# Kernel optimization log

Measured on AMD Instinct MI355X. Metric: run time of the kernel, lower is better.

The kernel has to match this reference:

```python
import jax, jax.numpy as jnp
import numpy as np

B, T, IN_DIM, EMBED, OUT_DIM, WS = 32, 512, 2048, 512, 29, 64


def setup_inputs() -> dict:
    key = jax.random.key(0)
    ks = jax.random.split(key, 8)
    x = jax.random.normal(ks[0], (B, T, IN_DIM), dtype=jnp.float32)
    # pack_padded_sequence contract: lengths sorted descending, max length == T
    lens = jnp.sort(jax.random.randint(ks[1], (B,), T // 2, T + 1))[::-1]
    sample_lengths = lens.at[0].set(T).astype(jnp.int64)
    s_in = 1.0 / np.sqrt(IN_DIM)
    s_q = 1.0 / np.sqrt(OUT_DIM)
    s_o = 1.0 / np.sqrt(EMBED)
    return {
        "x": x,
        "sample_lengths": sample_lengths,
        "W_in": jax.random.normal(ks[2], (IN_DIM, EMBED), jnp.float32) * s_in,
        "b_in": jnp.zeros((EMBED,), jnp.float32),
        "W_q": jax.random.normal(ks[3], (OUT_DIM, EMBED), jnp.float32) * s_q,
        "b_q": jnp.zeros((EMBED,), jnp.float32),
        "W_out": jax.random.normal(ks[4], (EMBED, OUT_DIM), jnp.float32) * s_o,
        "b_out": jnp.zeros((OUT_DIM,), jnp.float32),
        "window_size": WS,
    }


def reference(x, sample_lengths, W_in, b_in, W_q, b_q, W_out, b_out, window_size):
    # x: [B, T, input_dim] padded (pad_packed_sequence equivalent)
    Bb, Tt, _ = x.shape
    D = W_in.shape[1]
    h = x @ W_in + b_in                       # input_proj, [B, T, D]
    lens = sample_lengths
    j = jnp.arange(Tt)
    scale = 1.0 / jnp.sqrt(jnp.asarray(D, h.dtype))
    neg = jnp.finfo(h.dtype).min
    # generate_query0 with init_strategy='fix': ones, last channel = 9
    q0 = jnp.ones((Bb, 1, W_q.shape[0]), h.dtype).at[:, :, -1].set(9.0)

    def step(query, t):
        q = query @ W_q + b_q                 # query_proj, [B, 1, D]
        scores = jnp.einsum('bod,btd->bot', q, h) * scale  # [B, 1, T]
        # local window around query index t, clipped to each sequence length
        valid = (j >= t - window_size) & (j <= t + window_size) & (j[None, :] < lens[:, None])
        w = jax.nn.softmax(jnp.where(valid[:, None, :], scores, neg), axis=-1)
        alive = (t < lens).astype(h.dtype)[:, None, None]  # finished seqs -> zeros (blank_out/blank_wgts)
        out = jnp.einsum('bot,btd->bod', w, h) * alive      # [B, 1, D]
        new_query = out @ W_out + b_out        # output_proj, [B, 1, 29]
        return new_query, (new_query[:, 0, :], (w * alive)[:, 0, :])

    _, (outs, wgts) = jax.lax.scan(step, q0, jnp.arange(Tt))
    outputs = jnp.transpose(outs, (1, 0, 2))   # [B, T, 29]
    weights = jnp.transpose(wgts, (1, 0, 2))   # [B, T, T]
    return outputs, weights
```

## Files before the change

### kernel.cpp

```cpp
#include <hip/hip_runtime.h>
#include <math.h>

#define BB 32
#define TT 512
#define IND 2048
#define DD 512
#define OD 29
#define WCOLS 64
#define GC 32
#define PTK 116
#define PTB 18560

typedef float v2f __attribute__((ext_vector_type(2)));

__device__ __forceinline__ v2f pk_fma(v2f a, v2f b, v2f c) {
  v2f d;
  asm("v_pk_fma_f32 %0, %1, %2, %3" : "=v"(d) : "v"(a), "v"(b), "v"(c));
  return d;
}

template<int CTRL, int RM>
__device__ __forceinline__ float updpp(float idv, float x) {
  return __int_as_float(__builtin_amdgcn_update_dpp(
      __float_as_int(idv), __float_as_int(x), CTRL, RM, 0xf, false));
}

__device__ __forceinline__ float red_max64(float x) {
  const float ID = -3.0e38f;
  x = fmaxf(x, updpp<0xB1, 0xf>(ID, x));
  x = fmaxf(x, updpp<0x4E, 0xf>(ID, x));
  x = fmaxf(x, updpp<0x124, 0xf>(ID, x));
  x = fmaxf(x, updpp<0x128, 0xf>(ID, x));
  x = fmaxf(x, updpp<0x142, 0xa>(ID, x));
  x = fmaxf(x, updpp<0x143, 0xc>(ID, x));
  return __int_as_float(__builtin_amdgcn_readlane(__float_as_int(x), 63));
}

__device__ __forceinline__ float red_sum64(float x) {
  x += updpp<0xB1, 0xf>(0.f, x);
  x += updpp<0x4E, 0xf>(0.f, x);
  x += updpp<0x124, 0xf>(0.f, x);
  x += updpp<0x128, 0xf>(0.f, x);
  x += updpp<0x142, 0xa>(0.f, x);
  x += updpp<0x143, 0xc>(0.f, x);
  return __int_as_float(__builtin_amdgcn_readlane(__float_as_int(x), 63));
}

__global__ void k_zero(float* __restrict__ p, int n) {
  int n4 = n >> 2;
  int i = blockIdx.x * blockDim.x + threadIdx.x;
  int stride = gridDim.x * blockDim.x;
  float4 z = make_float4(0.f, 0.f, 0.f, 0.f);
  for (int j = i; j < n4; j += stride) ((float4*)p)[j] = z;
  int base = (n4 << 2) + i;
  if (base < n) p[base] = 0.f;
}

__global__ __launch_bounds__(64) void k_transform(
    const float* __restrict__ W_in, const float* __restrict__ b_in,
    const float* __restrict__ W_q,  const float* __restrict__ b_q,
    const float* __restrict__ W_out, float* __restrict__ Wt) {
  int i = blockIdx.x;
  int c = threadIdx.x;
  const float* row = (i < IND) ? (W_in + (size_t)i * DD) : b_in;
  const float* m;
  int strd;
  bool valid = true, dscale = false;
  if (c < OD)                { m = W_q + (size_t)c * DD; strd = 1; dscale = true; }
  else if (c == OD)          { m = b_q;                  strd = 1; dscale = true; }
  else if (c >= 32 && c < 32 + OD) { m = W_out + (c - 32); strd = OD; }
  else                       { m = b_q; strd = 0; valid = false; }
  float a0 = 0.f, a1 = 0.f, a2 = 0.f, a3 = 0.f;
  for (int d = 0; d < DD; d += 4) {
    a0 += row[d + 0] * m[(size_t)(d + 0) * strd];
    a1 += row[d + 1] * m[(size_t)(d + 1) * strd];
    a2 += row[d + 2] * m[(size_t)(d + 2) * strd];
    a3 += row[d + 3] * m[(size_t)(d + 3) * strd];
  }
  float acc = (a0 + a1) + (a2 + a3);
  if (dscale) acc *= (1.0f / sqrtf((float)DD));
  if (!valid) acc = 0.f;
  Wt[(size_t)i * WCOLS + c] = acc;
}

__global__ __launch_bounds__(256) void k_gemm(
    const float* __restrict__ x, const float* __restrict__ Wt,
    float* __restrict__ GPC, float* __restrict__ Ptg) {
  __shared__ float xt[128][65];
  int tid = threadIdx.x;
  int r = tid & 63;
  int cg16 = __builtin_amdgcn_readfirstlane((tid >> 6) << 4);
  int m0 = blockIdx.x << 6;
  int lr = tid >> 2, lc = tid & 3;
  const float* xl = x + (size_t)(m0 + lr) * IND;
  float4 a0 = make_float4(0,0,0,0), a1 = a0, a2 = a0, a3 = a0;
  for (int kk = 0; kk < IND; kk += 128) {
    __syncthreads();
    #pragma unroll
    for (int j = 0; j < 8; ++j) {
      int k = (lc + 4 * j) << 2;
      float4 v = *(const float4*)(xl + kk + k);
      xt[k + 0][lr] = v.x; xt[k + 1][lr] = v.y;
      xt[k + 2][lr] = v.z; xt[k + 3][lr] = v.w;
    }
    __syncthreads();
    const float* wb = Wt + (size_t)kk * WCOLS + cg16;
    #pragma unroll 4
    for (int k = 0; k < 128; ++k) {
      float xv = xt[k][r];
      const float* wk = wb + (size_t)k * WCOLS;
      float4 w0 = *(const float4*)(wk + 0);
      float4 w1 = *(const float4*)(wk + 4);
      float4 w2 = *(const float4*)(wk + 8);
      float4 w3 = *(const float4*)(wk + 12);
      a0.x += xv * w0.x; a0.y += xv * w0.y; a0.z += xv * w0.z; a0.w += xv * w0.w;
      a1.x += xv * w1.x; a1.y += xv * w1.y; a1.z += xv * w1.z; a1.w += xv * w1.w;
      a2.x += xv * w2.x; a2.y += xv * w2.y; a2.z += xv * w2.z; a2.w += xv * w2.w;
      a3.x += xv * w3.x; a3.y += xv * w3.y; a3.z += xv * w3.z; a3.w += xv * w3.w;
    }
  }
  const float* br = Wt + (size_t)IND * WCOLS + cg16;
  float4 b0 = *(const float4*)(br + 0), b1 = *(const float4*)(br + 4);
  float4 b2 = *(const float4*)(br + 8), b3 = *(const float4*)(br + 12);
  a0.x += b0.x; a0.y += b0.y; a0.z += b0.z; a0.w += b0.w;
  a1.x += b1.x; a1.y += b1.y; a1.z += b1.z; a1.w += b1.w;
  a2.x += b2.x; a2.y += b2.y; a2.z += b2.z; a2.w += b2.w;
  a3.x += b3.x; a3.y += b3.y; a3.z += b3.z; a3.w += b3.w;
  if (cg16 < 32) {
    float* o = GPC + (size_t)(m0 + r) * GC + cg16;
    *(float4*)(o + 0) = a0; *(float4*)(o + 4) = a1;
    *(float4*)(o + 8) = a2; *(float4*)(o + 12) = a3;
  } else {
    int bb = m0 >> 9;
    int jj = (m0 & 511) + r;
    int c0 = cg16 - 32;
    float va[16] = {a0.x,a0.y,a0.z,a0.w, a1.x,a1.y,a1.z,a1.w,
                    a2.x,a2.y,a2.z,a2.w, a3.x,a3.y,a3.z,a3.w};
    float* pb = Ptg + (size_t)bb * PTB + (size_t)(jj >> 2) * PTK + (jj & 3);
    #pragma unroll
    for (int cc = 0; cc < 16; ++cc)
      if (c0 + cc < OD) pb[(size_t)(c0 + cc) * 4] = va[cc];
  }
}

__device__ __forceinline__ void ld_g(v2f* g, const float* gb, int j) {
  const float4* s = (const float4*)(gb + (size_t)j * GC);
  #pragma unroll
  for (int u = 0; u < 8; ++u) {
    float4 v = s[u];
    g[2*u+0] = (v2f){v.x, v.y};
    g[2*u+1] = (v2f){v.z, v.w};
  }
}

__device__ __forceinline__ float score_pk(const v2f* g, const v2f* qp) {
  v2f a0 = pk_fma(qp[0], g[0], (v2f){0.f, 0.f});
  v2f a1 = pk_fma(qp[1], g[1], (v2f){0.f, 0.f});
  v2f a2 = pk_fma(qp[2], g[2], (v2f){0.f, 0.f});
  #pragma unroll
  for (int i = 3; i < 15; i += 3) {
    a0 = pk_fma(qp[i+0], g[i+0], a0);
    a1 = pk_fma(qp[i+1], g[i+1], a1);
    a2 = pk_fma(qp[i+2], g[i+2], a2);
  }
  v2f s = a0 + a1;
  s = s + a2;
  return s.x + s.y;
}

__global__ __launch_bounds__(64, 1) void k_scan(
    const float* __restrict__ GPC, const float* __restrict__ Ptg,
    const int* __restrict__ lens_raw,
    const float* __restrict__ b_out, const int* __restrict__ wsp,
    float* __restrict__ outputs, float* __restrict__ weights) {
  __shared__ __align__(16) float w_lds[640];

  int b = blockIdx.x;
  int l = threadIdx.x;
  int len;
  {
    int probe = lens_raw[1];
    len = (probe == 0) ? lens_raw[2 * b] : lens_raw[b];
  }
  if (len > TT) len = TT;
  if (len < 0) len = 0;
  int ws = wsp[0];

  const float* gb = GPC + (size_t)b * TT * GC;
  for (int j = l; j < 640; j += 64) w_lds[j] = 0.f;
  __syncthreads();

  int k = l & 31, h = l >> 5;
  int kc = (k < OD) ? k : (OD - 1);
  const float* pvK = Ptg + (size_t)b * PTB + kc * 4;
  float boutk = (k < OD) ? b_out[k] : 0.f;

  float* outb = outputs + (size_t)b * TT * OD;
  float* wb   = weights + (size_t)b * TT * TT;

  v2f qp[15];
  #pragma unroll
  for (int i = 0; i < 14; ++i) qp[i] = (v2f){1.f, 1.f};
  qp[14] = (v2f){9.f, 1.f};

  v2f g0[16], g1[16], g2[16];
  int j0r = l, j1r = 64 + l, j2r = 128 + l;
  ld_g(g0, gb, j0r); ld_g(g1, gb, j1r); ld_g(g2, gb, j2r);

  int jlo = 0;
  int jhi = (ws < len - 1) ? ws : (len - 1);

  float m_run = -3.0e38f;
  int t = 0;
  for (; t < len; ++t) {
    int qb = jlo >> 2;
    float4 rp[17];
    {
      const float* pr = pvK + (size_t)(qb + h) * PTK;
      #pragma unroll
      for (int i = 0; i < 17; ++i) rp[i] = *(const float4*)(pr + (size_t)(2 * i) * PTK);
    }
    __builtin_amdgcn_sched_barrier(0);
    float s0 = score_pk(g0, qp);
    float s1 = score_pk(g1, qp);
    float s2 = score_pk(g2, qp);
    bool v0 = (j0r >= jlo) & (j0r <= jhi);
    bool v1 = (j1r >= jlo) & (j1r <= jhi);
    bool v2 = (j2r >= jlo) & (j2r <= jhi);
    const float NEG = -3.0e38f;
    float mx0 = fmaxf(fmaxf(v0 ? s0 : NEG, v1 ? s1 : NEG), v2 ? s2 : NEG);
    float mx = m_run;
    float e0 = v0 ? __expf(s0 - mx) : 0.f;
    float e1 = v1 ? __expf(s1 - mx) : 0.f;
    float e2 = v2 ? __expf(s2 - mx) : 0.f;
    if (!(__all(mx0 <= m_run + 8.0f) && __any(mx0 >= m_run - 20.0f))) {
      mx = red_max64(mx0);
      m_run = mx;
      e0 = v0 ? __expf(s0 - mx) : 0.f;
      e1 = v1 ? __expf(s1 - mx) : 0.f;
      e2 = v2 ? __expf(s2 - mx) : 0.f;
    }
    if (l == 0 && jlo > 0) w_lds[jlo - 1] = 0.f;
    if (v0) w_lds[j0r] = e0;
    if (v1) w_lds[j1r] = e1;
    if (v2) w_lds[j2r] = e2;
    float sm = red_sum64(e0 + e1 + e2);
    float invS = __builtin_amdgcn_rcpf(sm);
    float* wrow = wb + (size_t)t * TT;
    if (v0) wrow[j0r] = e0 * invS;
    if (v1) wrow[j1r] = e1 * invS;
    if (v2) wrow[j2r] = e2 * invS;
    v2f pA = (v2f){0.f, 0.f}, pB = (v2f){0.f, 0.f};
    v2f pC = (v2f){0.f, 0.f}, pD = (v2f){0.f, 0.f};
    {
      const float* wr = w_lds + ((qb + h) << 2);
      #pragma unroll
      for (int i = 0; i < 17; i += 2) {
        float4 wv = *(const float4*)(wr + (i << 3));
        pA = pk_fma((v2f){wv.x, wv.y}, (v2f){rp[i].x, rp[i].y}, pA);
        pB = pk_fma((v2f){wv.z, wv.w}, (v2f){rp[i].z, rp[i].w}, pB);
      }
      #pragma unroll
      for (int i = 1; i < 17; i += 2) {
        float4 wv = *(const float4*)(wr + (i << 3));
        pC = pk_fma((v2f){wv.x, wv.y}, (v2f){rp[i].x, rp[i].y}, pC);
        pD = pk_fma((v2f){wv.z, wv.w}, (v2f){rp[i].z, rp[i].w}, pD);
      }
    }
    v2f ps = (pA + pC) + (pB + pD);
    float tot = ps.x + ps.y;
    float tc = tot;
    asm("v_permlane32_swap_b32 %0, %1" : "+v"(tot), "+v"(tc));
    float comb = tot + tc;
    float nq = comb * invS + boutk;
    if (h == 0 && k < OD) outb[(size_t)t * OD + k] = nq;
    #pragma unroll
    for (int kk = 0; kk < 14; ++kk) {
      float lo = __int_as_float(__builtin_amdgcn_readlane(__float_as_int(nq), 2*kk));
      float hi = __int_as_float(__builtin_amdgcn_readlane(__float_as_int(nq), 2*kk+1));
      qp[kk] = (v2f){lo, hi};
    }
    qp[14] = (v2f){__int_as_float(__builtin_amdgcn_readlane(__float_as_int(nq), 28)), 1.0f};
    int jnew = t + 2 + ws;
    if (jnew >= 192 && jnew < TT) {
      int sl = (jnew >> 6) % 3;
      int ln = jnew & 63;
      if (sl == 0)      { if (l == ln) { ld_g(g0, gb, jnew); j0r = jnew; } }
      else if (sl == 1) { if (l == ln) { ld_g(g1, gb, jnew); j1r = jnew; } }
      else              { if (l == ln) { ld_g(g2, gb, jnew); j2r = jnew; } }
    }
    jlo = (t + 1) - ws; if (jlo < 0) jlo = 0;
    jhi = (t + 1) + ws; if (jhi > len - 1) jhi = len - 1;
  }
  for (; t < TT; ++t)
    if (l < OD) outb[(size_t)t * OD + l] = boutk;
}

extern "C" void kernel_launch(void* const* d_in, const int* in_sizes, int n_in,
                              void* d_out, int out_size, void* d_ws, size_t ws_size,
                              hipStream_t stream) {
  const float* x     = (const float*)d_in[0];
  const int*   lens  = (const int*)d_in[1];
  const float* W_in  = (const float*)d_in[2];
  const float* b_in  = (const float*)d_in[3];
  const float* W_q   = (const float*)d_in[4];
  const float* b_q   = (const float*)d_in[5];
  const float* W_out = (const float*)d_in[6];
  const float* b_out = (const float*)d_in[7];
  const int*   wsp   = (const int*)d_in[8];
  float* out = (float*)d_out;

  float* Wt  = (float*)d_ws;
  float* GPC = Wt + (size_t)(IND + 1) * WCOLS;
  float* Ptg = GPC + (size_t)BB * TT * GC;

  k_zero<<<1024, 256, 0, stream>>>(out, out_size);
  k_zero<<<512, 256, 0, stream>>>(Ptg, BB * PTB);
  k_transform<<<IND + 1, 64, 0, stream>>>(W_in, b_in, W_q, b_q, W_out, Wt);
  k_gemm<<<(BB * TT) / 64, 256, 0, stream>>>(x, Wt, GPC, Ptg);

  float* outputs = out;
  float* weights = out + (size_t)BB * TT * OD;
  k_scan<<<BB, 64, 0, stream>>>(GPC, Ptg, lens, b_out, wsp, outputs, weights);
}
```

Measured before the change: 812.6 us.

## Double-buffer GEMM x tiles, use packed FMA, merge zero kernels

```diff
diff --git a/kernel.cpp b/kernel.cpp
--- a/kernel.cpp
+++ b/kernel.cpp
@@ -46,14 +46,16 @@
   return __int_as_float(__builtin_amdgcn_readlane(__float_as_int(x), 63));
 }
 
-__global__ void k_zero(float* __restrict__ p, int n) {
-  int n4 = n >> 2;
+__global__ void k_zero2(float* __restrict__ p1, int n1,
+                        float* __restrict__ p2, int n2) {
   int i = blockIdx.x * blockDim.x + threadIdx.x;
   int stride = gridDim.x * blockDim.x;
   float4 z = make_float4(0.f, 0.f, 0.f, 0.f);
-  for (int j = i; j < n4; j += stride) ((float4*)p)[j] = z;
-  int base = (n4 << 2) + i;
-  if (base < n) p[base] = 0.f;
+  int n14 = n1 >> 2, n24 = n2 >> 2;
+  for (int j = i; j < n14; j += stride) ((float4*)p1)[j] = z;
+  for (int j = i; j < n24; j += stride) ((float4*)p2)[j] = z;
+  int b1 = (n14 << 2) + i; if (b1 < n1) p1[b1] = 0.f;
+  int b2 = (n24 << 2) + i; if (b2 < n2) p2[b2] = 0.f;
 }
 
 __global__ __launch_bounds__(64) void k_transform(
@@ -86,39 +88,60 @@
 __global__ __launch_bounds__(256) void k_gemm(
     const float* __restrict__ x, const float* __restrict__ Wt,
     float* __restrict__ GPC, float* __restrict__ Ptg) {
-  __shared__ float xt[128][65];
+  __shared__ float xt[2][128][65];
   int tid = threadIdx.x;
   int r = tid & 63;
   int cg16 = __builtin_amdgcn_readfirstlane((tid >> 6) << 4);
   int m0 = blockIdx.x << 6;
   int lr = tid >> 2, lc = tid & 3;
   const float* xl = x + (size_t)(m0 + lr) * IND;
-  float4 a0 = make_float4(0,0,0,0), a1 = a0, a2 = a0, a3 = a0;
+  v2f acc[8];
+  #pragma unroll
+  for (int i = 0; i < 8; ++i) acc[i] = (v2f){0.f, 0.f};
+  #pragma unroll
+  for (int j = 0; j < 8; ++j) {
+    int k = (lc + 4 * j) << 2;
+    float4 v = *(const float4*)(xl + k);
+    xt[0][k + 0][lr] = v.x; xt[0][k + 1][lr] = v.y;
+    xt[0][k + 2][lr] = v.z; xt[0][k + 3][lr] = v.w;
+  }
+  __syncthreads();
   for (int kk = 0; kk < IND; kk += 128) {
-    __syncthreads();
-    #pragma unroll
-    for (int j = 0; j < 8; ++j) {
-      int k = (lc + 4 * j) << 2;
-      float4 v = *(const float4*)(xl + kk + k);
-      xt[k + 0][lr] = v.x; xt[k + 1][lr] = v.y;
-      xt[k + 2][lr] = v.z; xt[k + 3][lr] = v.w;
-    }
-    __syncthreads();
+    int cur = (kk >> 7) & 1;
+    if (kk + 128 < IND) {
+      #pragma unroll
+      for (int j = 0; j < 8; ++j) {
+        int k = (lc + 4 * j) << 2;
+        float4 v = *(const float4*)(xl + kk + 128 + k);
+        xt[cur ^ 1][k + 0][lr] = v.x; xt[cur ^ 1][k + 1][lr] = v.y;
+        xt[cur ^ 1][k + 2][lr] = v.z; xt[cur ^ 1][k + 3][lr] = v.w;
+      }
+    }
     const float* wb = Wt + (size_t)kk * WCOLS + cg16;
     #pragma unroll 4
     for (int k = 0; k < 128; ++k) {
-      float xv = xt[k][r];
+      float xv = xt[cur][k][r];
+      v2f xx = (v2f){xv, xv};
       const float* wk = wb + (size_t)k * WCOLS;
       float4 w0 = *(const float4*)(wk + 0);
       float4 w1 = *(const float4*)(wk + 4);
       float4 w2 = *(const float4*)(wk + 8);
       float4 w3 = *(const float4*)(wk + 12);
-      a0.x += xv * w0.x; a0.y += xv * w0.y; a0.z += xv * w0.z; a0.w += xv * w0.w;
-      a1.x += xv * w1.x; a1.y += xv * w1.y; a1.z += xv * w1.z; a1.w += xv * w1.w;
-      a2.x += xv * w2.x; a2.y += xv * w2.y; a2.z += xv * w2.z; a2.w += xv * w2.w;
-      a3.x += xv * w3.x; a3.y += xv * w3.y; a3.z += xv * w3.z; a3.w += xv * w3.w;
-    }
-  }
+      acc[0] = pk_fma(xx, (v2f){w0.x, w0.y}, acc[0]);
+      acc[1] = pk_fma(xx, (v2f){w0.z, w0.w}, acc[1]);
+      acc[2] = pk_fma(xx, (v2f){w1.x, w1.y}, acc[2]);
+      acc[3] = pk_fma(xx, (v2f){w1.z, w1.w}, acc[3]);
+      acc[4] = pk_fma(xx, (v2f){w2.x, w2.y}, acc[4]);
+      acc[5] = pk_fma(xx, (v2f){w2.z, w2.w}, acc[5]);
+      acc[6] = pk_fma(xx, (v2f){w3.x, w3.y}, acc[6]);
+      acc[7] = pk_fma(xx, (v2f){w3.z, w3.w}, acc[7]);
+    }
+    __syncthreads();
+  }
+  float4 a0 = make_float4(acc[0].x, acc[0].y, acc[1].x, acc[1].y);
+  float4 a1 = make_float4(acc[2].x, acc[2].y, acc[3].x, acc[3].y);
+  float4 a2 = make_float4(acc[4].x, acc[4].y, acc[5].x, acc[5].y);
+  float4 a3 = make_float4(acc[6].x, acc[6].y, acc[7].x, acc[7].y);
   const float* br = Wt + (size_t)IND * WCOLS + cg16;
   float4 b0 = *(const float4*)(br + 0), b1 = *(const float4*)(br + 4);
   float4 b2 = *(const float4*)(br + 8), b3 = *(const float4*)(br + 12);
@@ -314,12 +337,11 @@
   float* GPC = Wt + (size_t)(IND + 1) * WCOLS;
   float* Ptg = GPC + (size_t)BB * TT * GC;
 
-  k_zero<<<1024, 256, 0, stream>>>(out, out_size);
-  k_zero<<<512, 256, 0, stream>>>(Ptg, BB * PTB);
+  float* outputs = out;
+  float* weights = out + (size_t)BB * TT * OD;
+
+  k_zero2<<<1024, 256, 0, stream>>>(weights, BB * TT * TT, Ptg, BB * PTB);
   k_transform<<<IND + 1, 64, 0, stream>>>(W_in, b_in, W_q, b_q, W_out, Wt);
   k_gemm<<<(BB * TT) / 64, 256, 0, stream>>>(x, Wt, GPC, Ptg);
-
-  float* outputs = out;
-  float* weights = out + (size_t)BB * TT * OD;
   k_scan<<<BB, 64, 0, stream>>>(GPC, Ptg, lens, b_out, wsp, outputs, weights);
 }
```

After: 865.4 us. 6.5% more time.
